# Kernel optimization log

Measured on AMD Instinct MI355X. Metric: run time of the kernel, lower is better.

Reference implementation:

```python
import jax, jax.numpy as jnp
import numpy as np
from jax.scipy.linalg import solve_triangular

B, T, S, L, R, H = 64, 100, 32, 128, 16, 256

def bmv(A, v):
    return jnp.einsum('...ij,...j->...i', A, v)

def mT(A):
    return jnp.swapaxes(A, -1, -2)

def tri_inv_mT(chol):
    # Psi = inv(chol).T (upper triangular); chol is batched lower-triangular
    r = chol.shape[-1]
    I = jnp.broadcast_to(jnp.eye(r, dtype=chol.dtype), chol.shape)
    return mT(solve_triangular(chol, I, lower=True))

def chol_bmv_solve(Psi, v):
    # (chol chol^T)^{-1} v, using Psi = inv(chol)^T -> A^{-1} = Psi Psi^T
    return bmv(Psi, bmv(mT(Psi), v))

def filter_step_0(m_0, k0, K0, P_p_diag, w_p, w_f):
    # K0: (B,L,R); w_p: (S,B,L); w_f: (S,B,R)
    r = K0.shape[-1]
    z_p_c = jnp.sqrt(P_p_diag) * w_p
    m_p = jnp.broadcast_to(m_0, K0.shape[:1] + m_0.shape)  # (B,L)
    h = (1.0 / P_p_diag) * m_p + k0
    P_p_K = P_p_diag[None, :, None] * K0                    # (B,L,R)
    M = jnp.eye(r, dtype=K0.dtype) + mT(K0) @ P_p_K
    Psi = tri_inv_mT(jnp.linalg.cholesky(M))
    m = P_p_diag * h - bmv(P_p_K, chol_bmv_solve(Psi, bmv(mT(P_p_K), h)))
    v_1 = bmv(mT(K0), z_p_c) + w_f
    z = m + z_p_c - bmv(K0, chol_bmv_solve(Psi, v_1))
    return z, m

def predict_step(m_theta, Q_diag, w1, w2):
    # m_theta: (B,L,S) dynamics-mean particles
    s = m_theta.shape[-1]
    m_p = m_theta.mean(-1)                                   # (B,L)
    M_c = (m_theta - m_p[..., None]) * (1.0 / np.sqrt(s))    # (B,L,S)
    McT_Qinv = mT(M_c) * (1.0 / Q_diag)
    Psi_p = tri_inv_mT(jnp.linalg.cholesky(jnp.eye(s, dtype=m_theta.dtype) + McT_Qinv @ M_c))
    u1 = m_p / Q_diag
    u2 = (1.0 / Q_diag) * bmv(M_c, bmv(Psi_p, bmv(mT(Psi_p), bmv(mT(M_c), u1))))
    h_p = u1 - u2                                            # P_p^{-1} m_p (Woodbury)
    z_p_c = bmv(M_c, w1) + jnp.sqrt(Q_diag) * w2             # (S,B,L)
    return z_p_c, m_p, h_p, M_c

def update_step(z_p_c, h_p, k_t, K_t, w_f, M_c_p, Q_diag):
    r = K_t.shape[-1]
    Q_sqrt = jnp.sqrt(Q_diag)
    h = h_p + k_t
    K_M = mT(K_t) @ M_c_p                                    # (B,R,S)
    K_Q = mT(K_t) * Q_sqrt
    KPK = K_M @ mT(K_M) + K_Q @ mT(K_Q)                      # K^T P_p K
    Psi = tri_inv_mT(jnp.linalg.cholesky(jnp.eye(r, dtype=K_t.dtype) + KPK))
    P_p = lambda v: bmv(M_c_p, bmv(mT(M_c_p), v)) + Q_diag * v
    u1 = P_p(h)
    trip = bmv(K_t, bmv(Psi, bmv(mT(Psi), bmv(mT(K_t), u1))))
    m = u1 - P_p(trip)                                       # P_f h via Woodbury
    v_1 = bmv(mT(K_t), z_p_c) + w_f
    z = m + z_p_c - bmv(K_t, chol_bmv_solve(Psi, v_1))
    return m, z

def forward(k, K, m_0, P_p_diag, Q_diag, W1, W2, w_p0, w_f0, w_p1_seq, w_p2_seq, w_f_seq):
    mean_fn = lambda z: z + jnp.tanh(z @ W1) @ W2            # nonlinear dynamics mean
    k_tm = jnp.moveaxis(k, 1, 0)                              # (T,B,L)
    K_tm = jnp.moveaxis(K, 1, 0)                              # (T,B,L,R)
    z0, _ = filter_step_0(m_0, k_tm[0], K_tm[0], P_p_diag, w_p0, w_f0)

    def step(z_prev, inp):
        kt, Kt, w1, w2, wf = inp
        m_theta = jnp.moveaxis(mean_fn(z_prev), 0, -1)        # (B,L,S)
        z_p_c, m_p, h_p, M_c = predict_step(m_theta, Q_diag, w1, w2)
        m_f, z_f = update_step(z_p_c, h_p, kt, Kt, wf, M_c, Q_diag)
        return z_f, z_f

    _, zs = jax.lax.scan(step, z0, (k_tm[1:], K_tm[1:], w_p1_seq, w_p2_seq, w_f_seq))
    return jnp.concatenate([z0[None], zs], axis=0)            # (T,S,B,L)

def setup_inputs() -> dict:
    key = jax.random.key(0)
    ks = jax.random.split(key, 12)
    return {
        'k': 0.5 * jax.random.normal(ks[0], (B, T, L), jnp.float32),
        'K': 0.2 * jax.random.normal(ks[1], (B, T, L, R), jnp.float32),
        'm_0': jax.random.normal(ks[2], (L,), jnp.float32),
        'P_p_diag': jax.random.uniform(ks[3], (L,), jnp.float32, 0.5, 1.5),
        'Q_diag': jax.random.uniform(ks[4], (L,), jnp.float32, 0.5, 1.5),
        'W1': 0.02 * jax.random.normal(ks[5], (L, H), jnp.float32),
        'W2': 0.02 * jax.random.normal(ks[6], (H, L), jnp.float32),
        'w_p0': jax.random.normal(ks[7], (S, B, L), jnp.float32),
        'w_f0': jax.random.normal(ks[8], (S, B, R), jnp.float32),
        'w_p1_seq': jax.random.normal(ks[9], (T - 1, S, B, S), jnp.float32),
        'w_p2_seq': jax.random.normal(ks[10], (T - 1, S, B, L), jnp.float32),
        'w_f_seq': jax.random.normal(ks[11], (T - 1, S, B, R), jnp.float32),
    }

def reference(k, K, m_0, P_p_diag, Q_diag, W1, W2, w_p0, w_f0, w_p1_seq, w_p2_seq, w_f_seq):
    return forward(k, K, m_0, P_p_diag, Q_diag, W1, W2, w_p0, w_f0, w_p1_seq, w_p2_seq, w_f_seq)
```

## Files before the change

kernel.cpp:

```cpp
#include <hip/hip_runtime.h>
#include <math.h>

#define B_ 64
#define T_ 100
#define S_ 32
#define L_ 128
#define R_ 16
#define H_ 256

__device__ __forceinline__ float dot4(float4 a, float4 b) {
  return a.x*b.x + a.y*b.y + a.z*b.z + a.w*b.w;
}
__device__ __forceinline__ void wave_fence() {
  asm volatile("s_waitcnt lgkmcnt(0)" ::: "memory");
  __builtin_amdgcn_wave_barrier();
}

__device__ __forceinline__ void chol16_inv(int lane, float (*C2)[17], float (*G)[17], float* rd) {
  float row[16];
  #pragma unroll
  for (int c = 0; c < 16; ++c) row[c] = (lane < 16) ? C2[lane][c] : 0.0f;
  float rdg = 0.0f;
  #pragma unroll
  for (int j = 0; j < 16; ++j) {
    float dsq = __shfl(row[j], j);
    float d = sqrtf(dsq);
    float inv = 1.0f / d;
    float cij = row[j] * inv;
    if (lane == j) { cij = d; rdg = inv; }
    row[j] = cij;
    float upd = (lane > j) ? (cij * inv) : 0.0f;
    #pragma unroll
    for (int c = j + 1; c < 16; ++c) {
      float cjc = __shfl(row[c], j);
      row[c] -= upd * cjc;
    }
  }
  if (lane < 16) {
    #pragma unroll
    for (int c = 0; c < 16; ++c) C2[lane][c] = row[c];
    rd[lane] = rdg;
  }
  wave_fence();
  if (lane < 16) {
    const int c = lane;
    float g[16];
    #pragma unroll
    for (int i = 0; i < 16; ++i) {
      float a = (i == c) ? 1.0f : 0.0f;
      #pragma unroll
      for (int j2 = 0; j2 < 16; ++j2) if (j2 < i) a -= C2[i][j2] * g[j2];
      g[i] = a * rd[i];
    }
    #pragma unroll
    for (int i = 0; i < 16; ++i) G[i][c] = (i >= c) ? g[i] : 0.0f;
  }
  wave_fence();
}

__device__ __forceinline__ void chol32_fs(int lane, float (*C)[33],
                                          const float* t1, float* xb) {
  float row[32];
  #pragma unroll
  for (int c = 0; c < 32; ++c) row[c] = (lane < 32) ? C[lane][c] : 0.0f;
  float rdg = 0.0f;
  #pragma unroll
  for (int j = 0; j < 32; ++j) {
    float dsq = __shfl(row[j], j);
    float d = sqrtf(dsq);
    float inv = 1.0f / d;
    float cij = row[j] * inv;
    if (lane == j) { cij = d; rdg = inv; }
    row[j] = cij;
    float upd = (lane > j) ? (cij * inv) : 0.0f;
    #pragma unroll
    for (int c = j + 1; c < 32; ++c) {
      float cjc = __shfl(row[c], j);
      row[c] -= upd * cjc;
    }
  }
  float acc = (lane < 32) ? t1[lane] : 0.0f;
  #pragma unroll
  for (int j = 0; j < 32; ++j) {
    float xj = __shfl(acc, j) * __shfl(rdg, j);
    if (lane == j) acc = xj;
    else if (lane > j) acc -= row[j] * xj;
  }
  if (lane < 32) {
    #pragma unroll
    for (int c = 0; c < 32; ++c) C[lane][c] = row[c];
  }
  wave_fence();
  float colT[32];
  #pragma unroll
  for (int j = 0; j < 32; ++j) colT[j] = (lane < 32) ? C[j][lane] : 0.0f;
  float acc2 = acc;
  float xi = 0.0f;
  #pragma unroll
  for (int j = 31; j >= 0; --j) {
    float xj = __shfl(acc2, j) * __shfl(rdg, j);
    if (lane == j) xi = xj;
    if (lane < j) acc2 -= colT[j] * xj;
  }
  if (lane < 32) xb[lane] = xi;
  wave_fence();
}

__global__ __launch_bounds__(1024) void filter_kernel(
    const float* __restrict__ kg,
    const float* __restrict__ Kg,
    const float* __restrict__ m0g,
    const float* __restrict__ Ppg,
    const float* __restrict__ Qg,
    const float* __restrict__ wp0,
    const float* __restrict__ wf0,
    const float* __restrict__ wp1s,
    const float* __restrict__ wp2s,
    const float* __restrict__ wfs,
    const float* __restrict__ W1,
    const float* __restrict__ W2,
    float* __restrict__ out)
{
  const int b = blockIdx.x;
  const int tid = threadIdx.x;

  __shared__ float zc[S_][132];
  __shared__ float Ab[S_][264];
  __shared__ float Mc[S_][132];
  __shared__ float McT[L_][33];
  __shared__ float zp[S_][132];
  __shared__ float KtT[R_][132];
  __shared__ float w1b[S_][36];
  __shared__ float wfb[S_][20];
  __shared__ float C32m[32][33];
  __shared__ float C2m[16][17];
  __shared__ float Gm[16][17];
  __shared__ float KMm[16][36];
  __shared__ float v1b[S_][20];
  __shared__ float yb[S_][20];
  __shared__ float xvb[S_][20];
  __shared__ float red[32][17];
  __shared__ float mp[L_], u1[L_], hv[L_], uu[L_], mv[L_], trp[L_], ktv[L_];
  __shared__ float Qv[L_], iQ[L_], sQ[L_], Ppv[L_], sPp[L_], m0v[L_];
  __shared__ float t1v[32], tPh[32], xbuf[32];
  __shared__ float ttv[16], ssv[16], rd16[16], y2v[16];

  if (tid < L_) {
    float q = Qg[tid];  Qv[tid] = q;  iQ[tid] = 1.0f / q;  sQ[tid] = sqrtf(q);
    float p = Ppg[tid]; Ppv[tid] = p; sPp[tid] = sqrtf(p);
    m0v[tid] = m0g[tid];
  }
  __syncthreads();

  {
    if (tid < 512) {
      const float* Ksrc = Kg + (size_t)b * T_ * L_ * R_;
      float4 v = *(const float4*)(Ksrc + tid * 4);
      int l = (tid * 4) >> 4, r = (tid * 4) & 15;
      KtT[r+0][l] = v.x; KtT[r+1][l] = v.y; KtT[r+2][l] = v.z; KtT[r+3][l] = v.w;
    }
    {
      int s = tid >> 5, l = (tid & 31) * 4;
      float4 w = *(const float4*)(wp0 + ((size_t)s * B_ + b) * L_ + l);
      float4 p = *(const float4*)&sPp[l];
      *(float4*)&zp[s][l] = make_float4(w.x*p.x, w.y*p.y, w.z*p.z, w.w*p.w);
    }
    if (tid < 512) { int s = tid >> 4, r = tid & 15;
      wfb[s][r] = wf0[((size_t)s * B_ + b) * R_ + r]; }
    __syncthreads();

    if (tid < 256) {
      int r1 = tid >> 4, r2 = tid & 15;
      if (r1 <= r2) {
        float acc = (r1 == r2) ? 1.0f : 0.0f;
        for (int lc = 0; lc < 32; ++lc) {
          float4 a = *(const float4*)&KtT[r1][lc*4];
          float4 c = *(const float4*)&KtT[r2][lc*4];
          float4 p = *(const float4*)&Ppv[lc*4];
          acc += a.x*c.x*p.x + a.y*c.y*p.y + a.z*c.z*p.z + a.w*c.w*p.w;
        }
        C2m[r1][r2] = acc; C2m[r2][r1] = acc;
      }
      if (tid < 128) hv[tid] = m0v[tid] / Ppv[tid] + kg[(size_t)b * T_ * L_ + tid];
    } else if (tid < 512) {
      int q2 = tid - 256, s = q2 >> 3, r = (q2 & 7) * 2;
      float a0 = wfb[s][r], a1 = wfb[s][r+1];
      for (int lc = 0; lc < 32; ++lc) {
        float4 zz = *(const float4*)&zp[s][lc*4];
        float4 ka = *(const float4*)&KtT[r][lc*4];
        float4 kb = *(const float4*)&KtT[r+1][lc*4];
        a0 += dot4(zz, ka); a1 += dot4(zz, kb);
      }
      v1b[s][r] = a0; v1b[s][r+1] = a1;
    }
    __syncthreads();
    if (tid < 64) chol16_inv(tid, C2m, Gm, rd16);
    __syncthreads();
    if (tid < 512) {
      { int r = tid & 15, g = tid >> 4;
        float4 a = *(const float4*)&KtT[r][g*4];
        float4 p = *(const float4*)&Ppv[g*4];
        float4 h4 = *(const float4*)&hv[g*4];
        red[g][r] = a.x*p.x*h4.x + a.y*p.y*h4.y + a.z*p.z*h4.z + a.w*p.w*h4.w; }
      { int s = tid >> 4, r = tid & 15;
        float a = 0;
        #pragma unroll
        for (int j = 0; j < 16; ++j) a += Gm[r][j] * v1b[s][j];
        yb[s][r] = a; }
    }
    __syncthreads();
    if (tid < 512) { int s = tid >> 4, r = tid & 15;
      float a = 0;
      #pragma unroll
      for (int j = 0; j < 16; ++j) a += Gm[j][r] * yb[s][j];
      xvb[s][r] = a; }
    if (tid < 64) {
      if (tid < 16) { float a = 0;
        #pragma unroll
        for (int g = 0; g < 32; ++g) a += red[g][tid];
        ttv[tid] = a; }
      wave_fence();
      if (tid < 16) { float a = 0;
        #pragma unroll
        for (int j = 0; j < 16; ++j) a += Gm[tid][j] * ttv[j];
        y2v[tid] = a; }
      wave_fence();
      if (tid < 16) { float a = 0;
        #pragma unroll
        for (int j = 0; j < 16; ++j) a += Gm[j][tid] * y2v[j];
        ssv[tid] = a; }
    }
    __syncthreads();
    if (tid < 128) {
      float a = hv[tid];
      #pragma unroll
      for (int r = 0; r < 16; ++r) a -= KtT[r][tid] * ssv[r];
      mv[tid] = Ppv[tid] * a;
    }
    __syncthreads();
    if (tid < 512) {
      int s = tid >> 4, l0 = (tid & 15) * 8;
      float acc[8] = {0,0,0,0,0,0,0,0};
      #pragma unroll
      for (int r = 0; r < 16; ++r) {
        float xr = xvb[s][r];
        float4 k1 = *(const float4*)&KtT[r][l0];
        float4 k2 = *(const float4*)&KtT[r][l0+4];
        acc[0] += k1.x*xr; acc[1] += k1.y*xr; acc[2] += k1.z*xr; acc[3] += k1.w*xr;
        acc[4] += k2.x*xr; acc[5] += k2.y*xr; acc[6] += k2.z*xr; acc[7] += k2.w*xr;
      }
      float4 o1, o2;
      o1.x = mv[l0+0] + zp[s][l0+0] - acc[0]; o1.y = mv[l0+1] + zp[s][l0+1] - acc[1];
      o1.z = mv[l0+2] + zp[s][l0+2] - acc[2]; o1.w = mv[l0+3] + zp[s][l0+3] - acc[3];
      o2.x = mv[l0+4] + zp[s][l0+4] - acc[4]; o2.y = mv[l0+5] + zp[s][l0+5] - acc[5];
      o2.z = mv[l0+6] + zp[s][l0+6] - acc[6]; o2.w = mv[l0+7] + zp[s][l0+7] - acc[7];
      *(float4*)&zc[s][l0] = o1; *(float4*)&zc[s][l0+4] = o2;
      float* orow = out + ((size_t)s * B_ + b) * L_ + l0;
      *(float4*)orow = o1; *(float4*)(orow + 4) = o2;
    }
    __syncthreads();
  }

  for (int t = 1; t < T_; ++t) {
    if (tid < 512) {
      const float* Ksrc = Kg + ((size_t)b * T_ + t) * L_ * R_;
      float4 v = *(const float4*)(Ksrc + tid * 4);
      int l = (tid * 4) >> 4, r = (tid * 4) & 15;
      KtT[r+0][l] = v.x; KtT[r+1][l] = v.y; KtT[r+2][l] = v.z; KtT[r+3][l] = v.w;
      int s = tid >> 4, rr = tid & 15;
      wfb[s][rr] = wfs[(((size_t)(t-1) * S_ + s) * B_ + b) * R_ + rr];
      if (tid < 128) ktv[tid] = kg[((size_t)b * T_ + t) * L_ + tid];
    } else {
      int e = (tid - 512) * 2, s = e >> 5, j = e & 31;
      float2 v = *(const float2*)(wp1s + (((size_t)(t-1) * S_ + s) * B_ + b) * S_ + j);
      w1b[s][j] = v.x; w1b[s][j+1] = v.y;
    }

    {
      int s = tid >> 5, h0 = (tid & 31) * 8;
      float acc[8] = {0,0,0,0,0,0,0,0};
      for (int lc = 0; lc < 32; ++lc) {
        float4 z4 = *(const float4*)&zc[s][lc*4];
        const float* wbase = W1 + (size_t)(lc*4) * H_ + h0;
        float zv[4] = {z4.x, z4.y, z4.z, z4.w};
        #pragma unroll
        for (int q = 0; q < 4; ++q) {
          float4 wa = *(const float4*)(wbase + q*H_);
          float4 wb = *(const float4*)(wbase + q*H_ + 4);
          float zq = zv[q];
          acc[0] += zq*wa.x; acc[1] += zq*wa.y; acc[2] += zq*wa.z; acc[3] += zq*wa.w;
          acc[4] += zq*wb.x; acc[5] += zq*wb.y; acc[6] += zq*wb.z; acc[7] += zq*wb.w;
        }
      }
      #pragma unroll
      for (int j = 0; j < 8; ++j) Ab[s][h0 + j] = tanhf(acc[j]);
    }
    __syncthreads();
    {
      int s = tid >> 5, l0 = (tid & 31) * 4;
      float acc[4] = {0,0,0,0};
      for (int hc = 0; hc < 64; ++hc) {
        float4 a4 = *(const float4*)&Ab[s][hc*4];
        const float* wbase = W2 + (size_t)(hc*4) * L_ + l0;
        float av[4] = {a4.x, a4.y, a4.z, a4.w};
        #pragma unroll
        for (int q = 0; q < 4; ++q) {
          float4 w = *(const float4*)(wbase + q*L_);
          float aq = av[q];
          acc[0] += aq*w.x; acc[1] += aq*w.y; acc[2] += aq*w.z; acc[3] += aq*w.w;
        }
      }
      float4 z4 = *(const float4*)&zc[s][l0];
      *(float4*)&Mc[s][l0] = make_float4(z4.x+acc[0], z4.y+acc[1], z4.z+acc[2], z4.w+acc[3]);
    }
    __syncthreads();
    if (tid < 128) {
      float m = 0;
      #pragma unroll 8
      for (int s = 0; s < 32; ++s) m += Mc[s][tid];
      m *= (1.0f / 32.0f);
      mp[tid] = m; u1[tid] = m * iQ[tid];
    }
    __syncthreads();
    {
      int s = tid >> 5, l0 = (tid & 31) * 4;
      float4 m4 = *(const float4*)&Mc[s][l0];
      float4 p4 = *(const float4*)&mp[l0];
      float4 q4 = *(const float4*)&iQ[l0];
      const float cs = 0.17677669529663687f;
      float4 v4 = make_float4((m4.x-p4.x)*cs, (m4.y-p4.y)*cs, (m4.z-p4.z)*cs, (m4.w-p4.w)*cs);
      *(float4*)&Mc[s][l0] = v4;
      *(float4*)&Ab[s][l0] = make_float4(v4.x*q4.x, v4.y*q4.y, v4.z*q4.z, v4.w*q4.w);
      McT[l0+0][s] = v4.x; McT[l0+1][s] = v4.y; McT[l0+2][s] = v4.z; McT[l0+3][s] = v4.w;
    }
    __syncthreads();
    {
      { int s1 = tid >> 5, s2 = tid & 31;
        if (s1 <= s2) {
          float acc = (s1 == s2) ? 1.0f : 0.0f;
          for (int lc = 0; lc < 32; ++lc) {
            float4 a = *(const float4*)&Ab[s1][lc*4];
            float4 c = *(const float4*)&Mc[s2][lc*4];
            acc += dot4(a, c);
          }
          C32m[s1][s2] = acc; C32m[s2][s1] = acc;
        } }
      if (tid < 512) { int r = tid >> 5, s = tid & 31;
        float acc = 0;
        for (int lc = 0; lc < 32; ++lc) {
          float4 kk = *(const float4*)&KtT[r][lc*4];
          float4 mm = *(const float4*)&Mc[s][lc*4];
          acc += dot4(kk, mm);
        }
        KMm[r][s] = acc;
      } else { int g = tid - 512, s = g >> 4, seg = g & 15;
        float4 m1 = *(const float4*)&Mc[s][seg*8];
        float4 m2 = *(const float4*)&Mc[s][seg*8+4];
        float4 a1 = *(const float4*)&u1[seg*8];
        float4 a2 = *(const float4*)&u1[seg*8+4];
        red[s][seg] = dot4(m1, a1) + dot4(m2, a2);
      }
      {
        int s = tid >> 5, l0 = (tid & 31) * 4;
        float a0=0, a1=0, a2=0, a3=0;
        for (int j = 0; j < 32; ++j) {
          float wj = w1b[s][j];
          float4 m4 = *(const float4*)&Mc[j][l0];
          a0 += m4.x*wj; a1 += m4.y*wj; a2 += m4.z*wj; a3 += m4.w*wj;
        }
        const float* w2src = wp2s + (((size_t)(t-1) * S_ + s) * B_ + b) * L_ + l0;
        float4 wv = *(const float4*)(w2src);
        float4 q4 = *(const float4*)&sQ[l0];
        *(float4*)&zp[s][l0] = make_float4(a0+q4.x*wv.x, a1+q4.y*wv.y, a2+q4.z*wv.z, a3+q4.w*wv.w);
      }
    }
    __syncthreads();
    if (tid < 256) {
      int r1 = tid >> 4, r2 = tid & 15;
      if (r1 <= r2) {
        float acc = (r1 == r2) ? 1.0f : 0.0f;
        #pragma unroll
        for (int sc2 = 0; sc2 < 8; ++sc2) {
          float4 a = *(const float4*)&KMm[r1][sc2*4];
          float4 c = *(const float4*)&KMm[r2][sc2*4];
          acc += dot4(a, c);
        }
        for (int lc = 0; lc < 32; ++lc) {
          float4 a = *(const float4*)&KtT[r1][lc*4];
          float4 c = *(const float4*)&KtT[r2][lc*4];
          float4 q = *(const float4*)&Qv[lc*4];
          acc += a.x*c.x*q.x + a.y*c.y*q.y + a.z*c.z*q.z + a.w*c.w*q.w;
        }
        C2m[r1][r2] = acc; C2m[r2][r1] = acc;
      }
    } else if (tid < 288) {
      int s = tid - 256;
      float a = 0;
      #pragma unroll
      for (int g = 0; g < 16; ++g) a += red[s][g];
      t1v[s] = a;
    } else if (tid >= 512) {
      int g = tid - 512, s = g >> 4, r = g & 15;
      float a = wfb[s][r];
      for (int lc = 0; lc < 32; ++lc) {
        float4 zz = *(const float4*)&zp[s][lc*4];
        float4 kk = *(const float4*)&KtT[r][lc*4];
        a += dot4(zz, kk);
      }
      v1b[s][r] = a;
    }
    __syncthreads();
    if (tid < 64) chol32_fs(tid, C32m, t1v, xbuf);
    else if (tid < 128) chol16_inv(tid - 64, C2m, Gm, rd16);
    __syncthreads();
    if (tid < 64) {
      const int ln = tid;
      const int l0 = ln, l1 = ln + 64;
      float a0 = 0.f, a1 = 0.f;
      for (int s = 0; s < 32; ++s) {
        float xs = xbuf[s];
        a0 += McT[l0][s] * xs; a1 += McT[l1][s] * xs;
      }
      hv[l0] = u1[l0] + ktv[l0] - iQ[l0] * a0;
      hv[l1] = u1[l1] + ktv[l1] - iQ[l1] * a1;
      wave_fence();
      {
        int s = ln & 31, hb = (ln >> 5) * 64;
        float p = 0;
        #pragma unroll
        for (int l = 0; l < 64; l += 4) {
          float4 m4 = *(const float4*)&Mc[s][hb+l];
          float4 h4 = *(const float4*)&hv[hb+l];
          p += dot4(m4, h4);
        }
        p += __shfl_xor(p, 32);
        if (ln < 32) tPh[s] = p;
      }
      wave_fence();
      a0 = 0.f; a1 = 0.f;
      for (int s = 0; s < 32; ++s) {
        float ts = tPh[s];
        a0 += McT[l0][s] * ts; a1 += McT[l1][s] * ts;
      }
      uu[l0] = Qv[l0]*hv[l0] + a0;
      uu[l1] = Qv[l1]*hv[l1] + a1;
      wave_fence();
      float ttr;
      { int r = ln & 15, qd = ln >> 4;
        float p = 0;
        #pragma unroll
        for (int l = 0; l < 32; l += 4) {
          float4 k4 = *(const float4*)&KtT[r][qd*32+l];
          float4 u4 = *(const float4*)&uu[qd*32+l];
          p += dot4(k4, u4);
        }
        p += __shfl_xor(p, 16);
        p += __shfl_xor(p, 32);
        ttr = p;
      }
      { int r = ln & 15;
        float y2 = 0;
        #pragma unroll
        for (int j = 0; j < 16; ++j) y2 += Gm[r][j] * __shfl(ttr, j);
        float ssr = 0;
        #pragma unroll
        for (int j = 0; j < 16; ++j) ssr += Gm[j][r] * __shfl(y2, j);
        if (ln < 16) ssv[r] = ssr;
      }
      wave_fence();
      a0 = 0.f; a1 = 0.f;
      #pragma unroll
      for (int r = 0; r < 16; ++r) {
        float sr = ssv[r];
        a0 += KtT[r][l0] * sr; a1 += KtT[r][l1] * sr;
      }
      trp[l0] = a0; trp[l1] = a1;
      wave_fence();
      {
        int s = ln & 31, hb = (ln >> 5) * 64;
        float p = 0;
        #pragma unroll
        for (int l = 0; l < 64; l += 4) {
          float4 m4 = *(const float4*)&Mc[s][hb+l];
          float4 h4 = *(const float4*)&trp[hb+l];
          p += dot4(m4, h4);
        }
        p += __shfl_xor(p, 32);
        if (ln < 32) tPh[s] = p;
      }
      wave_fence();
      a0 = 0.f; a1 = 0.f;
      for (int s = 0; s < 32; ++s) {
        float ts = tPh[s];
        a0 += McT[l0][s] * ts; a1 += McT[l1][s] * ts;
      }
      mv[l0] = uu[l0] - Qv[l0]*trp[l0] - a0;
      mv[l1] = uu[l1] - Qv[l1]*trp[l1] - a1;
    } else if (tid < 576) {
      int g = tid - 64;
      int s = g >> 4, r = g & 15;
      int sb = (g & 63) & 48;
      float yv = 0;
      #pragma unroll
      for (int j = 0; j < 16; ++j) yv += Gm[r][j] * v1b[s][j];
      float xr_ = 0;
      #pragma unroll
      for (int j = 0; j < 16; ++j) xr_ += Gm[j][r] * __shfl(yv, sb + j);
      float xl[16];
      #pragma unroll
      for (int j = 0; j < 16; ++j) xl[j] = __shfl(xr_, sb + j);
      int lb = r * 8;
      float acc[8] = {0,0,0,0,0,0,0,0};
      #pragma unroll
      for (int r2 = 0; r2 < 16; ++r2) {
        float xr = xl[r2];
        #pragma unroll
        for (int i = 0; i < 8; ++i) acc[i] += KtT[r2][lb+i] * xr;
      }
      float4 z1 = *(const float4*)&zp[s][lb];
      float4 z2 = *(const float4*)&zp[s][lb+4];
      z1.x -= acc[0]; z1.y -= acc[1]; z1.z -= acc[2]; z1.w -= acc[3];
      z2.x -= acc[4]; z2.y -= acc[5]; z2.z -= acc[6]; z2.w -= acc[7];
      *(float4*)&zp[s][lb] = z1; *(float4*)&zp[s][lb+4] = z2;
    }
    __syncthreads();
    {
      int s = tid >> 5, l0 = (tid & 31) * 4;
      float4 z4 = *(const float4*)&zp[s][l0];
      float4 m4 = *(const float4*)&mv[l0];
      z4.x += m4.x; z4.y += m4.y; z4.z += m4.z; z4.w += m4.w;
      *(float4*)&zc[s][l0] = z4;
      *(float4*)(out + (((size_t)t * S_ + s) * B_ + b) * L_ + l0) = z4;
    }
    __syncthreads();
  }
}

extern "C" void kernel_launch(void* const* d_in, const int* in_sizes, int n_in,
                              void* d_out, int out_size, void* d_ws, size_t ws_size,
                              hipStream_t stream) {
  const float* kg  = (const float*)d_in[0];
  const float* Kg  = (const float*)d_in[1];
  const float* m0  = (const float*)d_in[2];
  const float* Pp  = (const float*)d_in[3];
  const float* Qd  = (const float*)d_in[4];
  const float* W1  = (const float*)d_in[5];
  const float* W2  = (const float*)d_in[6];
  const float* wp0 = (const float*)d_in[7];
  const float* wf0 = (const float*)d_in[8];
  const float* wp1 = (const float*)d_in[9];
  const float* wp2 = (const float*)d_in[10];
  const float* wfs = (const float*)d_in[11];
  float* outp = (float*)d_out;
  (void)d_ws; (void)ws_size;

  filter_kernel<<<B_, 1024, 0, stream>>>(kg, Kg, m0, Pp, Qd, wp0, wf0,
                                         wp1, wp2, wfs, W1, W2, outp);
}
```

Before: 8.585 ms.

## Keep particle state in registers and fuse MLP via shuffles, dropping barriers

The current particle row now lives in registers (zr), so the zc buffer goes away. The two-layer MLP runs inside each 32-lane group using shuffles, which removes the Ab round-trip and a block barrier. The McT transpose is dropped in favour of strided reads of Mc. Per-step global loads are issued early into registers and written to shared memory later, and the z_p computation moves into its own phase. Several dot-product loops also get split accumulators for more ILP, at the cost of more register pressure in a 1024-thread block and a heavy shuffle count in the MLP.

```diff
diff --git a/kernel.cpp b/kernel.cpp
--- a/kernel.cpp
+++ b/kernel.cpp
@@ -123,11 +123,11 @@
 {
   const int b = blockIdx.x;
   const int tid = threadIdx.x;
-
-  __shared__ float zc[S_][132];
-  __shared__ float Ab[S_][264];
+  const int lane_l = tid & 31;
+  const int sp = tid >> 5;
+
+  __shared__ float Ab[S_][132];
   __shared__ float Mc[S_][132];
-  __shared__ float McT[L_][33];
   __shared__ float zp[S_][132];
   __shared__ float KtT[R_][132];
   __shared__ float w1b[S_][36];
@@ -145,6 +145,8 @@
   __shared__ float t1v[32], tPh[32], xbuf[32];
   __shared__ float ttv[16], ssv[16], rd16[16], y2v[16];
 
+  float4 zr;
+
   if (tid < L_) {
     float q = Qg[tid];  Qv[tid] = q;  iQ[tid] = 1.0f / q;  sQ[tid] = sqrtf(q);
     float p = Ppg[tid]; Ppv[tid] = p; sPp[tid] = sqrtf(p);
@@ -160,10 +162,10 @@
       KtT[r+0][l] = v.x; KtT[r+1][l] = v.y; KtT[r+2][l] = v.z; KtT[r+3][l] = v.w;
     }
     {
-      int s = tid >> 5, l = (tid & 31) * 4;
-      float4 w = *(const float4*)(wp0 + ((size_t)s * B_ + b) * L_ + l);
+      int l = lane_l * 4;
+      float4 w = *(const float4*)(wp0 + ((size_t)sp * B_ + b) * L_ + l);
       float4 p = *(const float4*)&sPp[l];
-      *(float4*)&zp[s][l] = make_float4(w.x*p.x, w.y*p.y, w.z*p.z, w.w*p.w);
+      *(float4*)&zp[sp][l] = make_float4(w.x*p.x, w.y*p.y, w.z*p.z, w.w*p.w);
     }
     if (tid < 512) { int s = tid >> 4, r = tid & 15;
       wfb[s][r] = wf0[((size_t)s * B_ + b) * R_ + r]; }
@@ -172,13 +174,14 @@
     if (tid < 256) {
       int r1 = tid >> 4, r2 = tid & 15;
       if (r1 <= r2) {
-        float acc = (r1 == r2) ? 1.0f : 0.0f;
+        float4 a4 = {0,0,0,0};
         for (int lc = 0; lc < 32; ++lc) {
           float4 a = *(const float4*)&KtT[r1][lc*4];
           float4 c = *(const float4*)&KtT[r2][lc*4];
           float4 p = *(const float4*)&Ppv[lc*4];
-          acc += a.x*c.x*p.x + a.y*c.y*p.y + a.z*c.z*p.z + a.w*c.w*p.w;
-        }
+          a4.x += a.x*c.x*p.x; a4.y += a.y*c.y*p.y; a4.z += a.z*c.z*p.z; a4.w += a.w*c.w*p.w;
+        }
+        float acc = a4.x+a4.y+a4.z+a4.w + ((r1 == r2) ? 1.0f : 0.0f);
         C2m[r1][r2] = acc; C2m[r2][r1] = acc;
       }
       if (tid < 128) hv[tid] = m0v[tid] / Ppv[tid] + kg[(size_t)b * T_ * L_ + tid];
@@ -238,121 +241,151 @@
       mv[tid] = Ppv[tid] * a;
     }
     __syncthreads();
+    {
+      int l0 = lane_l * 4;
+      float4 acc = {0,0,0,0};
+      #pragma unroll
+      for (int r = 0; r < 16; ++r) {
+        float xr = xvb[sp][r];
+        float4 k = *(const float4*)&KtT[r][l0];
+        acc.x += k.x*xr; acc.y += k.y*xr; acc.z += k.z*xr; acc.w += k.w*xr;
+      }
+      float4 m4 = *(const float4*)&mv[l0];
+      float4 z4 = *(const float4*)&zp[sp][l0];
+      zr.x = m4.x + z4.x - acc.x; zr.y = m4.y + z4.y - acc.y;
+      zr.z = m4.z + z4.z - acc.z; zr.w = m4.w + z4.w - acc.w;
+      *(float4*)(out + ((size_t)sp * B_ + b) * L_ + l0) = zr;
+    }
+    __syncthreads();
+  }
+
+  for (int t = 1; t < T_; ++t) {
+    float4 kst; float wfst = 0.f, ktst = 0.f; float2 w1st; float4 w2st;
+    {
+      const float* w2src = wp2s + (((size_t)(t-1) * S_ + sp) * B_ + b) * L_ + lane_l * 4;
+      w2st = *(const float4*)w2src;
+      if (tid < 512) {
+        const float* Ksrc = Kg + ((size_t)b * T_ + t) * L_ * R_;
+        kst = *(const float4*)(Ksrc + tid * 4);
+        wfst = wfs[(((size_t)(t-1) * S_ + (tid >> 4)) * B_ + b) * R_ + (tid & 15)];
+        if (tid < 128) ktst = kg[((size_t)b * T_ + t) * L_ + tid];
+      } else {
+        int e = (tid - 512) * 2;
+        w1st = *(const float2*)(wp1s + (((size_t)(t-1) * S_ + (e >> 5)) * B_ + b) * S_ + (e & 31));
+      }
+    }
+
+    {
+      float acc1[8] = {0,0,0,0,0,0,0,0};
+      #pragma unroll 2
+      for (int kq = 0; kq < 32; ++kq) {
+        float4 zk;
+        zk.x = __shfl(zr.x, kq, 32); zk.y = __shfl(zr.y, kq, 32);
+        zk.z = __shfl(zr.z, kq, 32); zk.w = __shfl(zr.w, kq, 32);
+        const float* wbase = W1 + (size_t)kq * 1024 + lane_l * 8;
+        float zv[4] = {zk.x, zk.y, zk.z, zk.w};
+        #pragma unroll
+        for (int q = 0; q < 4; ++q) {
+          float4 wa = *(const float4*)(wbase + q * H_);
+          float4 wb = *(const float4*)(wbase + q * H_ + 4);
+          float zq = zv[q];
+          acc1[0] += zq*wa.x; acc1[1] += zq*wa.y; acc1[2] += zq*wa.z; acc1[3] += zq*wa.w;
+          acc1[4] += zq*wb.x; acc1[5] += zq*wb.y; acc1[6] += zq*wb.z; acc1[7] += zq*wb.w;
+        }
+      }
+      float a8[8];
+      #pragma unroll
+      for (int j = 0; j < 8; ++j) a8[j] = tanhf(acc1[j]);
+      float4 acc2 = {0,0,0,0};
+      #pragma unroll 2
+      for (int hq = 0; hq < 32; ++hq) {
+        float av[8];
+        av[0] = __shfl(a8[0], hq, 32); av[1] = __shfl(a8[1], hq, 32);
+        av[2] = __shfl(a8[2], hq, 32); av[3] = __shfl(a8[3], hq, 32);
+        av[4] = __shfl(a8[4], hq, 32); av[5] = __shfl(a8[5], hq, 32);
+        av[6] = __shfl(a8[6], hq, 32); av[7] = __shfl(a8[7], hq, 32);
+        const float* wbase = W2 + (size_t)hq * 1024 + lane_l * 4;
+        #pragma unroll
+        for (int j = 0; j < 8; ++j) {
+          float4 w = *(const float4*)(wbase + j * L_);
+          float aq = av[j];
+          acc2.x += aq*w.x; acc2.y += aq*w.y; acc2.z += aq*w.z; acc2.w += aq*w.w;
+        }
+      }
+      float4 mth = make_float4(zr.x+acc2.x, zr.y+acc2.y, zr.z+acc2.z, zr.w+acc2.w);
+      *(float4*)&Mc[sp][lane_l*4] = mth;
+    }
+
     if (tid < 512) {
-      int s = tid >> 4, l0 = (tid & 15) * 8;
-      float acc[8] = {0,0,0,0,0,0,0,0};
-      #pragma unroll
-      for (int r = 0; r < 16; ++r) {
-        float xr = xvb[s][r];
-        float4 k1 = *(const float4*)&KtT[r][l0];
-        float4 k2 = *(const float4*)&KtT[r][l0+4];
-        acc[0] += k1.x*xr; acc[1] += k1.y*xr; acc[2] += k1.z*xr; acc[3] += k1.w*xr;
-        acc[4] += k2.x*xr; acc[5] += k2.y*xr; acc[6] += k2.z*xr; acc[7] += k2.w*xr;
-      }
-      float4 o1, o2;
-      o1.x = mv[l0+0] + zp[s][l0+0] - acc[0]; o1.y = mv[l0+1] + zp[s][l0+1] - acc[1];
-      o1.z = mv[l0+2] + zp[s][l0+2] - acc[2]; o1.w = mv[l0+3] + zp[s][l0+3] - acc[3];
-      o2.x = mv[l0+4] + zp[s][l0+4] - acc[4]; o2.y = mv[l0+5] + zp[s][l0+5] - acc[5];
-      o2.z = mv[l0+6] + zp[s][l0+6] - acc[6]; o2.w = mv[l0+7] + zp[s][l0+7] - acc[7];
-      *(float4*)&zc[s][l0] = o1; *(float4*)&zc[s][l0+4] = o2;
-      float* orow = out + ((size_t)s * B_ + b) * L_ + l0;
-      *(float4*)orow = o1; *(float4*)(orow + 4) = o2;
-    }
-    __syncthreads();
-  }
-
-  for (int t = 1; t < T_; ++t) {
-    if (tid < 512) {
-      const float* Ksrc = Kg + ((size_t)b * T_ + t) * L_ * R_;
-      float4 v = *(const float4*)(Ksrc + tid * 4);
       int l = (tid * 4) >> 4, r = (tid * 4) & 15;
-      KtT[r+0][l] = v.x; KtT[r+1][l] = v.y; KtT[r+2][l] = v.z; KtT[r+3][l] = v.w;
-      int s = tid >> 4, rr = tid & 15;
-      wfb[s][rr] = wfs[(((size_t)(t-1) * S_ + s) * B_ + b) * R_ + rr];
-      if (tid < 128) ktv[tid] = kg[((size_t)b * T_ + t) * L_ + tid];
+      KtT[r+0][l] = kst.x; KtT[r+1][l] = kst.y; KtT[r+2][l] = kst.z; KtT[r+3][l] = kst.w;
+      wfb[tid >> 4][tid & 15] = wfst;
+      if (tid < 128) ktv[tid] = ktst;
     } else {
-      int e = (tid - 512) * 2, s = e >> 5, j = e & 31;
-      float2 v = *(const float2*)(wp1s + (((size_t)(t-1) * S_ + s) * B_ + b) * S_ + j);
-      w1b[s][j] = v.x; w1b[s][j+1] = v.y;
-    }
-
-    {
-      int s = tid >> 5, h0 = (tid & 31) * 8;
-      float acc[8] = {0,0,0,0,0,0,0,0};
-      for (int lc = 0; lc < 32; ++lc) {
-        float4 z4 = *(const float4*)&zc[s][lc*4];
-        const float* wbase = W1 + (size_t)(lc*4) * H_ + h0;
-        float zv[4] = {z4.x, z4.y, z4.z, z4.w};
-        #pragma unroll
-        for (int q = 0; q < 4; ++q) {
-          float4 wa = *(const float4*)(wbase + q*H_);
-          float4 wb = *(const float4*)(wbase + q*H_ + 4);
-          float zq = zv[q];
-          acc[0] += zq*wa.x; acc[1] += zq*wa.y; acc[2] += zq*wa.z; acc[3] += zq*wa.w;
-          acc[4] += zq*wb.x; acc[5] += zq*wb.y; acc[6] += zq*wb.z; acc[7] += zq*wb.w;
-        }
-      }
-      #pragma unroll
-      for (int j = 0; j < 8; ++j) Ab[s][h0 + j] = tanhf(acc[j]);
-    }
-    __syncthreads();
-    {
-      int s = tid >> 5, l0 = (tid & 31) * 4;
-      float acc[4] = {0,0,0,0};
-      for (int hc = 0; hc < 64; ++hc) {
-        float4 a4 = *(const float4*)&Ab[s][hc*4];
-        const float* wbase = W2 + (size_t)(hc*4) * L_ + l0;
-        float av[4] = {a4.x, a4.y, a4.z, a4.w};
-        #pragma unroll
-        for (int q = 0; q < 4; ++q) {
-          float4 w = *(const float4*)(wbase + q*L_);
-          float aq = av[q];
-          acc[0] += aq*w.x; acc[1] += aq*w.y; acc[2] += aq*w.z; acc[3] += aq*w.w;
-        }
-      }
-      float4 z4 = *(const float4*)&zc[s][l0];
-      *(float4*)&Mc[s][l0] = make_float4(z4.x+acc[0], z4.y+acc[1], z4.z+acc[2], z4.w+acc[3]);
-    }
-    __syncthreads();
+      int e = (tid - 512) * 2;
+      w1b[e >> 5][e & 31] = w1st.x; w1b[e >> 5][(e & 31) + 1] = w1st.y;
+    }
+    __syncthreads();
+
     if (tid < 128) {
-      float m = 0;
-      #pragma unroll 8
-      for (int s = 0; s < 32; ++s) m += Mc[s][tid];
-      m *= (1.0f / 32.0f);
+      float a0=0, a1=0, a2=0, a3=0;
+      #pragma unroll
+      for (int s = 0; s < 32; s += 4) {
+        a0 += Mc[s][tid]; a1 += Mc[s+1][tid]; a2 += Mc[s+2][tid]; a3 += Mc[s+3][tid];
+      }
+      float m = (a0+a1+a2+a3) * (1.0f / 32.0f);
       mp[tid] = m; u1[tid] = m * iQ[tid];
     }
     __syncthreads();
-    {
-      int s = tid >> 5, l0 = (tid & 31) * 4;
-      float4 m4 = *(const float4*)&Mc[s][l0];
+
+    {
+      int l0 = lane_l * 4;
+      float4 m4 = *(const float4*)&Mc[sp][l0];
       float4 p4 = *(const float4*)&mp[l0];
       float4 q4 = *(const float4*)&iQ[l0];
       const float cs = 0.17677669529663687f;
       float4 v4 = make_float4((m4.x-p4.x)*cs, (m4.y-p4.y)*cs, (m4.z-p4.z)*cs, (m4.w-p4.w)*cs);
-      *(float4*)&Mc[s][l0] = v4;
-      *(float4*)&Ab[s][l0] = make_float4(v4.x*q4.x, v4.y*q4.y, v4.z*q4.z, v4.w*q4.w);
-      McT[l0+0][s] = v4.x; McT[l0+1][s] = v4.y; McT[l0+2][s] = v4.z; McT[l0+3][s] = v4.w;
-    }
-    __syncthreads();
+      *(float4*)&Mc[sp][l0] = v4;
+      *(float4*)&Ab[sp][l0] = make_float4(v4.x*q4.x, v4.y*q4.y, v4.z*q4.z, v4.w*q4.w);
+    }
+    __syncthreads();
+
+    {
+      float wrow = w1b[sp][lane_l];
+      float4 az = {0,0,0,0};
+      #pragma unroll 4
+      for (int j = 0; j < 32; ++j) {
+        float wj = __shfl(wrow, j, 32);
+        float4 m4 = *(const float4*)&Mc[j][lane_l*4];
+        az.x += wj*m4.x; az.y += wj*m4.y; az.z += wj*m4.z; az.w += wj*m4.w;
+      }
+      int l0 = lane_l * 4;
+      float4 q4 = *(const float4*)&sQ[l0];
+      *(float4*)&zp[sp][l0] = make_float4(az.x + q4.x*w2st.x, az.y + q4.y*w2st.y,
+                                          az.z + q4.z*w2st.z, az.w + q4.w*w2st.w);
+    }
+    __syncthreads();
+
     {
       { int s1 = tid >> 5, s2 = tid & 31;
         if (s1 <= s2) {
-          float acc = (s1 == s2) ? 1.0f : 0.0f;
+          float4 a4 = {0,0,0,0};
           for (int lc = 0; lc < 32; ++lc) {
             float4 a = *(const float4*)&Ab[s1][lc*4];
             float4 c = *(const float4*)&Mc[s2][lc*4];
-            acc += dot4(a, c);
+            a4.x += a.x*c.x; a4.y += a.y*c.y; a4.z += a.z*c.z; a4.w += a.w*c.w;
           }
+          float acc = a4.x+a4.y+a4.z+a4.w + ((s1 == s2) ? 1.0f : 0.0f);
           C32m[s1][s2] = acc; C32m[s2][s1] = acc;
         } }
       if (tid < 512) { int r = tid >> 5, s = tid & 31;
-        float acc = 0;
+        float4 a4 = {0,0,0,0};
         for (int lc = 0; lc < 32; ++lc) {
           float4 kk = *(const float4*)&KtT[r][lc*4];
           float4 mm = *(const float4*)&Mc[s][lc*4];
-          acc += dot4(kk, mm);
-        }
-        KMm[r][s] = acc;
+          a4.x += kk.x*mm.x; a4.y += kk.y*mm.y; a4.z += kk.z*mm.z; a4.w += kk.w*mm.w;
+        }
+        KMm[r][s] = a4.x+a4.y+a4.z+a4.w;
       } else { int g = tid - 512, s = g >> 4, seg = g & 15;
         float4 m1 = *(const float4*)&Mc[s][seg*8];
         float4 m2 = *(const float4*)&Mc[s][seg*8+4];
@@ -360,37 +393,26 @@
         float4 a2 = *(const float4*)&u1[seg*8+4];
         red[s][seg] = dot4(m1, a1) + dot4(m2, a2);
       }
-      {
-        int s = tid >> 5, l0 = (tid & 31) * 4;
-        float a0=0, a1=0, a2=0, a3=0;
-        for (int j = 0; j < 32; ++j) {
-          float wj = w1b[s][j];
-          float4 m4 = *(const float4*)&Mc[j][l0];
-          a0 += m4.x*wj; a1 += m4.y*wj; a2 += m4.z*wj; a3 += m4.w*wj;
-        }
-        const float* w2src = wp2s + (((size_t)(t-1) * S_ + s) * B_ + b) * L_ + l0;
-        float4 wv = *(const float4*)(w2src);
-        float4 q4 = *(const float4*)&sQ[l0];
-        *(float4*)&zp[s][l0] = make_float4(a0+q4.x*wv.x, a1+q4.y*wv.y, a2+q4.z*wv.z, a3+q4.w*wv.w);
-      }
-    }
-    __syncthreads();
+    }
+    __syncthreads();
+
     if (tid < 256) {
       int r1 = tid >> 4, r2 = tid & 15;
       if (r1 <= r2) {
-        float acc = (r1 == r2) ? 1.0f : 0.0f;
+        float4 a4 = {0,0,0,0};
         #pragma unroll
         for (int sc2 = 0; sc2 < 8; ++sc2) {
           float4 a = *(const float4*)&KMm[r1][sc2*4];
           float4 c = *(const float4*)&KMm[r2][sc2*4];
-          acc += dot4(a, c);
+          a4.x += a.x*c.x; a4.y += a.y*c.y; a4.z += a.z*c.z; a4.w += a.w*c.w;
         }
         for (int lc = 0; lc < 32; ++lc) {
           float4 a = *(const float4*)&KtT[r1][lc*4];
           float4 c = *(const float4*)&KtT[r2][lc*4];
           float4 q = *(const float4*)&Qv[lc*4];
-          acc += a.x*c.x*q.x + a.y*c.y*q.y + a.z*c.z*q.z + a.w*c.w*q.w;
-        }
+          a4.x += a.x*c.x*q.x; a4.y += a.y*c.y*q.y; a4.z += a.z*c.z*q.z; a4.w += a.w*c.w*q.w;
+        }
+        float acc = a4.x+a4.y+a4.z+a4.w + ((r1 == r2) ? 1.0f : 0.0f);
         C2m[r1][r2] = acc; C2m[r2][r1] = acc;
       }
     } else if (tid < 288) {
@@ -401,59 +423,71 @@
       t1v[s] = a;
     } else if (tid >= 512) {
       int g = tid - 512, s = g >> 4, r = g & 15;
-      float a = wfb[s][r];
+      float4 a4 = {0,0,0,0};
       for (int lc = 0; lc < 32; ++lc) {
         float4 zz = *(const float4*)&zp[s][lc*4];
         float4 kk = *(const float4*)&KtT[r][lc*4];
-        a += dot4(zz, kk);
-      }
-      v1b[s][r] = a;
-    }
-    __syncthreads();
+        a4.x += zz.x*kk.x; a4.y += zz.y*kk.y; a4.z += zz.z*kk.z; a4.w += zz.w*kk.w;
+      }
+      v1b[s][r] = wfb[s][r] + a4.x+a4.y+a4.z+a4.w;
+    }
+    __syncthreads();
+
     if (tid < 64) chol32_fs(tid, C32m, t1v, xbuf);
     else if (tid < 128) chol16_inv(tid - 64, C2m, Gm, rd16);
     __syncthreads();
+
     if (tid < 64) {
       const int ln = tid;
       const int l0 = ln, l1 = ln + 64;
-      float a0 = 0.f, a1 = 0.f;
-      for (int s = 0; s < 32; ++s) {
-        float xs = xbuf[s];
-        a0 += McT[l0][s] * xs; a1 += McT[l1][s] * xs;
-      }
-      hv[l0] = u1[l0] + ktv[l0] - iQ[l0] * a0;
-      hv[l1] = u1[l1] + ktv[l1] - iQ[l1] * a1;
+      float p0=0,p1=0,p2=0,p3=0, q0=0,q1=0,q2=0,q3=0;
+      #pragma unroll
+      for (int s = 0; s < 32; s += 4) {
+        float x0 = xbuf[s], x1 = xbuf[s+1], x2 = xbuf[s+2], x3 = xbuf[s+3];
+        p0 += Mc[s][l0]*x0; p1 += Mc[s+1][l0]*x1; p2 += Mc[s+2][l0]*x2; p3 += Mc[s+3][l0]*x3;
+        q0 += Mc[s][l1]*x0; q1 += Mc[s+1][l1]*x1; q2 += Mc[s+2][l1]*x2; q3 += Mc[s+3][l1]*x3;
+      }
+      hv[l0] = u1[l0] + ktv[l0] - iQ[l0] * (p0+p1+p2+p3);
+      hv[l1] = u1[l1] + ktv[l1] - iQ[l1] * (q0+q1+q2+q3);
       wave_fence();
       {
         int s = ln & 31, hb = (ln >> 5) * 64;
-        float p = 0;
-        #pragma unroll
-        for (int l = 0; l < 64; l += 4) {
-          float4 m4 = *(const float4*)&Mc[s][hb+l];
-          float4 h4 = *(const float4*)&hv[hb+l];
-          p += dot4(m4, h4);
-        }
+        float pa = 0, pb = 0;
+        #pragma unroll
+        for (int l = 0; l < 64; l += 8) {
+          float4 m1 = *(const float4*)&Mc[s][hb+l];
+          float4 h1 = *(const float4*)&hv[hb+l];
+          float4 m2 = *(const float4*)&Mc[s][hb+l+4];
+          float4 h2 = *(const float4*)&hv[hb+l+4];
+          pa += dot4(m1, h1); pb += dot4(m2, h2);
+        }
+        float p = pa + pb;
         p += __shfl_xor(p, 32);
         if (ln < 32) tPh[s] = p;
       }
       wave_fence();
-      a0 = 0.f; a1 = 0.f;
-      for (int s = 0; s < 32; ++s) {
-        float ts = tPh[s];
-        a0 += McT[l0][s] * ts; a1 += McT[l1][s] * ts;
-      }
-      uu[l0] = Qv[l0]*hv[l0] + a0;
-      uu[l1] = Qv[l1]*hv[l1] + a1;
+      p0=0;p1=0;p2=0;p3=0;q0=0;q1=0;q2=0;q3=0;
+      #pragma unroll
+      for (int s = 0; s < 32; s += 4) {
+        float x0 = tPh[s], x1 = tPh[s+1], x2 = tPh[s+2], x3 = tPh[s+3];
+        p0 += Mc[s][l0]*x0; p1 += Mc[s+1][l0]*x1; p2 += Mc[s+2][l0]*x2; p3 += Mc[s+3][l0]*x3;
+        q0 += Mc[s][l1]*x0; q1 += Mc[s+1][l1]*x1; q2 += Mc[s+2][l1]*x2; q3 += Mc[s+3][l1]*x3;
+      }
+      uu[l0] = Qv[l0]*hv[l0] + (p0+p1+p2+p3);
+      uu[l1] = Qv[l1]*hv[l1] + (q0+q1+q2+q3);
       wave_fence();
       float ttr;
       { int r = ln & 15, qd = ln >> 4;
-        float p = 0;
-        #pragma unroll
-        for (int l = 0; l < 32; l += 4) {
-          float4 k4 = *(const float4*)&KtT[r][qd*32+l];
+        float pa = 0, pb = 0;
+        #pragma unroll
+        for (int l = 0; l < 32; l += 8) {
+          float4 k1 = *(const float4*)&KtT[r][qd*32+l];
           float4 u4 = *(const float4*)&uu[qd*32+l];
-          p += dot4(k4, u4);
-        }
+          float4 k2 = *(const float4*)&KtT[r][qd*32+l+4];
+          float4 u5 = *(const float4*)&uu[qd*32+l+4];
+          pa += dot4(k1, u4); pb += dot4(k2, u5);
+        }
+        float p = pa + pb;
         p += __shfl_xor(p, 16);
         p += __shfl_xor(p, 32);
         ttr = p;
@@ -468,38 +502,43 @@
         if (ln < 16) ssv[r] = ssr;
       }
       wave_fence();
-      a0 = 0.f; a1 = 0.f;
-      #pragma unroll
-      for (int r = 0; r < 16; ++r) {
-        float sr = ssv[r];
-        a0 += KtT[r][l0] * sr; a1 += KtT[r][l1] * sr;
-      }
-      trp[l0] = a0; trp[l1] = a1;
+      { float a0 = 0, a1 = 0;
+        #pragma unroll
+        for (int r = 0; r < 16; ++r) {
+          float sr = ssv[r];
+          a0 += KtT[r][l0] * sr; a1 += KtT[r][l1] * sr;
+        }
+        trp[l0] = a0; trp[l1] = a1; }
       wave_fence();
       {
         int s = ln & 31, hb = (ln >> 5) * 64;
-        float p = 0;
-        #pragma unroll
-        for (int l = 0; l < 64; l += 4) {
-          float4 m4 = *(const float4*)&Mc[s][hb+l];
-          float4 h4 = *(const float4*)&trp[hb+l];
-          p += dot4(m4, h4);
-        }
+        float pa = 0, pb = 0;
+        #pragma unroll
+        for (int l = 0; l < 64; l += 8) {
+          float4 m1 = *(const float4*)&Mc[s][hb+l];
+          float4 h1 = *(const float4*)&trp[hb+l];
+          float4 m2 = *(const float4*)&Mc[s][hb+l+4];
+          float4 h2 = *(const float4*)&trp[hb+l+4];
+          pa += dot4(m1, h1); pb += dot4(m2, h2);
+        }
+        float p = pa + pb;
         p += __shfl_xor(p, 32);
         if (ln < 32) tPh[s] = p;
       }
       wave_fence();
-      a0 = 0.f; a1 = 0.f;
-      for (int s = 0; s < 32; ++s) {
-        float ts = tPh[s];
-        a0 += McT[l0][s] * ts; a1 += McT[l1][s] * ts;
-      }
-      mv[l0] = uu[l0] - Qv[l0]*trp[l0] - a0;
-      mv[l1] = uu[l1] - Qv[l1]*trp[l1] - a1;
+      p0=0;p1=0;p2=0;p3=0;q0=0;q1=0;q2=0;q3=0;
+      #pragma unroll
+      for (int s = 0; s < 32; s += 4) {
+        float x0 = tPh[s], x1 = tPh[s+1], x2 = tPh[s+2], x3 = tPh[s+3];
+        p0 += Mc[s][l0]*x0; p1 += Mc[s+1][l0]*x1; p2 += Mc[s+2][l0]*x2; p3 += Mc[s+3][l0]*x3;
+        q0 += Mc[s][l1]*x0; q1 += Mc[s+1][l1]*x1; q2 += Mc[s+2][l1]*x2; q3 += Mc[s+3][l1]*x3;
+      }
+      mv[l0] = uu[l0] - Qv[l0]*trp[l0] - (p0+p1+p2+p3);
+      mv[l1] = uu[l1] - Qv[l1]*trp[l1] - (q0+q1+q2+q3);
     } else if (tid < 576) {
       int g = tid - 64;
       int s = g >> 4, r = g & 15;
-      int sb = (g & 63) & 48;
+      int sb = g & 48;
       float yv = 0;
       #pragma unroll
       for (int j = 0; j < 16; ++j) yv += Gm[r][j] * v1b[s][j];
@@ -510,29 +549,30 @@
       #pragma unroll
       for (int j = 0; j < 16; ++j) xl[j] = __shfl(xr_, sb + j);
       int lb = r * 8;
-      float acc[8] = {0,0,0,0,0,0,0,0};
+      float4 ac1 = {0,0,0,0}, ac2 = {0,0,0,0};
       #pragma unroll
       for (int r2 = 0; r2 < 16; ++r2) {
         float xr = xl[r2];
-        #pragma unroll
-        for (int i = 0; i < 8; ++i) acc[i] += KtT[r2][lb+i] * xr;
+        float4 k1 = *(const float4*)&KtT[r2][lb];
+        float4 k2 = *(const float4*)&KtT[r2][lb+4];
+        ac1.x += xr*k1.x; ac1.y += xr*k1.y; ac1.z += xr*k1.z; ac1.w += xr*k1.w;
+        ac2.x += xr*k2.x; ac2.y += xr*k2.y; ac2.z += xr*k2.z; ac2.w += xr*k2.w;
       }
       float4 z1 = *(const float4*)&zp[s][lb];
       float4 z2 = *(const float4*)&zp[s][lb+4];
-      z1.x -= acc[0]; z1.y -= acc[1]; z1.z -= acc[2]; z1.w -= acc[3];
-      z2.x -= acc[4]; z2.y -= acc[5]; z2.z -= acc[6]; z2.w -= acc[7];
+      z1.x -= ac1.x; z1.y -= ac1.y; z1.z -= ac1.z; z1.w -= ac1.w;
+      z2.x -= ac2.x; z2.y -= ac2.y; z2.z -= ac2.z; z2.w -= ac2.w;
       *(float4*)&zp[s][lb] = z1; *(float4*)&zp[s][lb+4] = z2;
     }
     __syncthreads();
-    {
-      int s = tid >> 5, l0 = (tid & 31) * 4;
-      float4 z4 = *(const float4*)&zp[s][l0];
+
+    {
+      int l0 = lane_l * 4;
+      float4 z4 = *(const float4*)&zp[sp][l0];
       float4 m4 = *(const float4*)&mv[l0];
-      z4.x += m4.x; z4.y += m4.y; z4.z += m4.z; z4.w += m4.w;
-      *(float4*)&zc[s][l0] = z4;
-      *(float4*)(out + (((size_t)t * S_ + s) * B_ + b) * L_ + l0) = z4;
-    }
-    __syncthreads();
+      zr.x = z4.x + m4.x; zr.y = z4.y + m4.y; zr.z = z4.z + m4.z; zr.w = z4.w + m4.w;
+      *(float4*)(out + (((size_t)t * S_ + sp) * B_ + b) * L_ + l0) = zr;
+    }
   }
 }
 
```

Measured after the change: 8.762 ms. +2.1%, slower.
